# Performance work log

Measured on AMD Instinct MI355X. Metric: run time of the kernel, lower is better.

## Reference

```python
import jax, jax.numpy as jnp
import numpy as np

B, S, E = 2, 2048, 2048
H, KV, D = 16, 4, 128


def setup_inputs() -> dict:
    key = jax.random.key(0)
    k0, k1, k2, k3, k4 = jax.random.split(key, 5)
    s = 0.02  # init scale for weights
    return {
        "x": jax.random.normal(k0, (B, S, E), jnp.float32),
        "wq": jax.random.normal(k1, (E, H * D), jnp.float32) * s,
        "wk": jax.random.normal(k2, (E, KV * D), jnp.float32) * s,
        "wv": jax.random.normal(k3, (E, KV * D), jnp.float32) * s,
        "wo": jax.random.normal(k4, (H * D, E), jnp.float32) * s,
    }


def _rope_tables(seq_len, head_dim, dtype):
    inv_freq = 1.0 / (10000.0 ** (jnp.arange(0, head_dim, 2, dtype=jnp.float32) / head_dim))
    t = jnp.arange(seq_len, dtype=jnp.float32)
    freqs = jnp.outer(t, inv_freq)  # [S, D/2]
    emb = jnp.concatenate([freqs, freqs], axis=-1)  # [S, D]
    cos = jnp.cos(emb).astype(dtype)[None, None]  # [1,1,S,D]
    sin = jnp.sin(emb).astype(dtype)[None, None]
    return cos, sin


def _rotate_half(x):
    x1, x2 = jnp.split(x, 2, axis=-1)
    return jnp.concatenate([-x2, x1], axis=-1)


def reference(x, wq, wk, wv, wo):
    b, s, _ = x.shape
    # projections -> [B, heads, S, D]
    q = (x @ wq).reshape(b, s, H, D).transpose(0, 2, 1, 3)
    k = (x @ wk).reshape(b, s, KV, D).transpose(0, 2, 1, 3)
    v = (x @ wv).reshape(b, s, KV, D).transpose(0, 2, 1, 3)
    # inline RoPE (rotate-half convention), applied to q and k
    cos, sin = _rope_tables(s, D, q.dtype)
    q = q * cos + _rotate_half(q) * sin
    k = k * cos + _rotate_half(k) * sin
    # GQA: duplicate K/V heads (repeat_interleave along head dim)
    rep = H // KV
    k = jnp.repeat(k, rep, axis=1)
    v = jnp.repeat(v, rep, axis=1)
    scale = 1.0 / np.sqrt(D)
    scores = jnp.einsum('bhqd,bhkd->bhqk', q, k) * scale  # [B,H,S,S]
    attn = jax.nn.softmax(scores.astype(jnp.float32), axis=-1).astype(q.dtype)
    out = jnp.einsum('bhqk,bhkd->bhqd', attn, v)  # [B,H,S,D]
    out = out.transpose(0, 2, 1, 3).reshape(b, s, H * D)
    return out @ wo
```

## Files before the change

### kernel.cpp

```cpp
#include <hip/hip_runtime.h>
#include <hip/hip_bf16.h>

typedef __attribute__((ext_vector_type(8))) short s16x8;
typedef __attribute__((ext_vector_type(4))) float f32x4;

__device__ inline float bf2f(unsigned short u) {
  union { unsigned int i; float f; } v; v.i = ((unsigned int)u) << 16; return v.f;
}
__device__ inline unsigned short f2bf(float f) {
  union { float f; unsigned int i; } v; v.f = f;
  unsigned int r = (v.i + 0x7FFFu + ((v.i >> 16) & 1u)) >> 16;
  return (unsigned short)r;
}
__device__ inline void gl_lds16(const void* g, void* l) {
  __builtin_amdgcn_global_load_lds(
      (const __attribute__((address_space(1))) unsigned int*)g,
      (__attribute__((address_space(3))) unsigned int*)l, 16, 0, 0);
}

__global__ __launch_bounds__(256) void cast_to_bf16(const float* __restrict__ s,
                                                    unsigned short* __restrict__ d, int n4) {
  int i = blockIdx.x * 256 + threadIdx.x;
  if (i >= n4) return;
  float4 v = ((const float4*)s)[i];
  ushort4 o;
  o.x = f2bf(v.x); o.y = f2bf(v.y); o.z = f2bf(v.z); o.w = f2bf(v.w);
  ((ushort4*)d)[i] = o;
}

__global__ __launch_bounds__(256) void transpose_cast(const float* __restrict__ src,
                                                      unsigned short* __restrict__ dst,
                                                      int K, int N) {
  __shared__ float tile[32][33];
  int n0 = blockIdx.x * 32, k0 = blockIdx.y * 32;
  int tx = threadIdx.x & 31, ty = threadIdx.x >> 5;
#pragma unroll
  for (int i = 0; i < 4; ++i) {
    int k = ty + i * 8;
    tile[k][tx] = src[(size_t)(k0 + k) * N + n0 + tx];
  }
  __syncthreads();
#pragma unroll
  for (int i = 0; i < 4; ++i) {
    int n = ty + i * 8;
    dst[(size_t)(n0 + n) * K + k0 + tx] = f2bf(tile[tx][n]);
  }
}

__global__ __launch_bounds__(256) void rope_tables(float* __restrict__ ct, float* __restrict__ st) {
  int idx = blockIdx.x * 256 + threadIdx.x;
  int s = idx >> 6, i = idx & 63;
  float inv = powf(10000.0f, -(float)(2 * i) * (1.0f / 128.0f));
  float ang = (float)s * inv;
  ct[idx] = cosf(ang);
  st[idx] = sinf(ang);
}

__global__ __launch_bounds__(256) void rope_apply(unsigned short* __restrict__ qkv,
                                                  const float* __restrict__ ct,
                                                  const float* __restrict__ st) {
  int row = blockIdx.x;
  int pos = row & 2047;
  unsigned short* base = qkv + (size_t)row * 3072;
  for (int it = threadIdx.x; it < 1280; it += 256) {
    int head = it >> 6, dh = it & 63;
    int col = head < 16 ? head * 128 : 2048 + (head - 16) * 128;
    float a = bf2f(base[col + dh]);
    float b = bf2f(base[col + dh + 64]);
    float c = ct[pos * 64 + dh], sn = st[pos * 64 + dh];
    base[col + dh] = f2bf(a * c - b * sn);
    base[col + dh + 64] = f2bf(b * c + a * sn);
  }
}

__global__ __launch_bounds__(256) void vtrans(const unsigned short* __restrict__ qkv,
                                              unsigned short* __restrict__ vt) {
  __shared__ unsigned short tile[32][33];
  int tx = threadIdx.x & 31, ty = threadIdx.x >> 5;
  int s0 = blockIdx.x * 32;
  int d0 = blockIdx.y * 32;
  int bz = blockIdx.z;
  const unsigned short* src = qkv + (size_t)((bz >> 2) * 2048) * 3072 + 2560 + (bz & 3) * 128;
#pragma unroll
  for (int i = 0; i < 4; ++i)
    tile[ty + i * 8][tx] = src[(size_t)(s0 + ty + i * 8) * 3072 + d0 + tx];
  __syncthreads();
  unsigned short* dst = vt + (size_t)bz * 128 * 2048;
#pragma unroll
  for (int i = 0; i < 4; ++i)
    dst[(size_t)(d0 + ty + i * 8) * 2048 + s0 + tx] = tile[tx][ty + i * 8];
}

template <int BF16OUT>
__global__ __launch_bounds__(512, 2) void gemm256(const unsigned short* __restrict__ A,
                                                  const unsigned short* __restrict__ BT,
                                                  void* __restrict__ Cv,
                                                  int M, int N, int K) {
  __shared__ __align__(16) unsigned short Lds[2][4][256 * 32];
  const int t = threadIdx.x, lane = t & 63;
  const int wid = t >> 6, m16 = lane & 15, l4 = lane >> 4;
  const int wm = wid >> 2, wn = wid & 3;
  const int swA = (l4 ^ ((m16 >> 1) & 3)) * 16;

  int gx = gridDim.x, nwg = gx * gridDim.y;
  int wg = blockIdx.y * gx + blockIdx.x;
  if ((nwg & 7) == 0) { int q = nwg >> 3; wg = (wg & 7) * q + (wg >> 3); }
  const int rowBase = (wg / gx) * 256, colBase = (wg % gx) * 256;

  const int r0 = t >> 2, c80 = (t & 3) ^ ((r0 >> 1) & 3);
  const int g1 = 512 + t, r1 = g1 >> 2, c81 = (g1 & 3) ^ ((r1 >> 1) & 3);
  const char* pA0 = (const char*)(A + (size_t)(rowBase + r0) * K + c80 * 8);
  const char* pA1 = (const char*)(A + (size_t)(rowBase + r1) * K + c81 * 8);
  const char* pB0 = (const char*)(BT + (size_t)(colBase + r0) * K + c80 * 8);
  const char* pB1 = (const char*)(BT + (size_t)(colBase + r1) * K + c81 * 8);

  f32x4 acc[8][4];
#pragma unroll
  for (int fr = 0; fr < 8; ++fr)
#pragma unroll
    for (int fn = 0; fn < 4; ++fn) {
      f32x4 z = {0.f, 0.f, 0.f, 0.f};
      acc[fr][fn] = z;
    }
  s16x8 bf[4];

#define STG(mat, kc, kt, buf)                                             \
  {                                                                       \
    size_t ko = (size_t)((kt) * 64 + (kc) * 32) * 2;                      \
    char* pl = (char*)&Lds[buf][(mat) * 2 + (kc)][0];                     \
    gl_lds16(((mat) ? pB0 : pA0) + ko, pl + t * 16);                      \
    gl_lds16(((mat) ? pB1 : pA1) + ko, pl + 8192 + t * 16);               \
  }

#define GATE()                                         \
  asm volatile("s_waitcnt vmcnt(8)" ::: "memory");     \
  __builtin_amdgcn_s_barrier();                        \
  __builtin_amdgcn_sched_barrier(0);

#define CMP(cur, kc, frh)                                                          \
  {                                                                                \
    const char* Ap = (const char*)&Lds[cur][kc][0];                                \
    s16x8 af[4];                                                                   \
    _Pragma("unroll") for (int i = 0; i < 4; ++i)                                  \
        af[i] = *(const s16x8*)(Ap + (wm * 128 + ((frh) * 4 + i) * 16 + m16) * 64 + swA); \
    if ((frh) == 0) {                                                              \
      const char* Bp = (const char*)&Lds[cur][2 + (kc)][0];                        \
      _Pragma("unroll") for (int n = 0; n < 4; ++n)                                \
          bf[n] = *(const s16x8*)(Bp + (wn * 64 + n * 16 + m16) * 64 + swA);       \
    }                                                                              \
    __builtin_amdgcn_s_setprio(1);                                                 \
    _Pragma("unroll") for (int i = 0; i < 4; ++i)                                  \
        _Pragma("unroll") for (int n = 0; n < 4; ++n)                              \
            acc[(frh) * 4 + i][n] = __builtin_amdgcn_mfma_f32_16x16x32_bf16(       \
                af[i], bf[n], acc[(frh) * 4 + i][n], 0, 0, 0);                     \
    __builtin_amdgcn_s_setprio(0);                                                 \
  }

  const int NT = K >> 6;
  STG(0, 0, 0, 0); STG(1, 0, 0, 0);
  STG(0, 1, 0, 0); STG(1, 1, 0, 0);
  STG(0, 0, 1, 1); STG(1, 0, 1, 1);

  for (int kt = 0; kt < NT; ++kt) {
    const int cur = kt & 1;
    GATE();
    if (kt + 1 < NT) STG(0, 1, kt + 1, cur ^ 1);
    CMP(cur, 0, 0);
    __builtin_amdgcn_s_barrier();
    if (kt + 1 < NT) STG(1, 1, kt + 1, cur ^ 1);
    CMP(cur, 0, 1);
    GATE();
    if (kt + 2 < NT) STG(0, 0, kt + 2, cur);
    CMP(cur, 1, 0);
    __builtin_amdgcn_s_barrier();
    if (kt + 2 < NT) STG(1, 0, kt + 2, cur);
    CMP(cur, 1, 1);
  }
#undef STG
#undef GATE
#undef CMP

#pragma unroll
  for (int fr = 0; fr < 8; ++fr)
#pragma unroll
    for (int fn = 0; fn < 4; ++fn) {
      int rr = rowBase + wm * 128 + fr * 16 + l4 * 4;
      int cc = colBase + wn * 64 + fn * 16 + m16;
#pragma unroll
      for (int jr = 0; jr < 4; ++jr) {
        if (BF16OUT)
          ((unsigned short*)Cv)[(size_t)(rr + jr) * N + cc] = f2bf(acc[fr][fn][jr]);
        else
          ((float*)Cv)[(size_t)(rr + jr) * N + cc] = acc[fr][fn][jr];
      }
    }
}

__global__ __launch_bounds__(256, 2) void attn_kernel(const unsigned short* __restrict__ qkv,
                                                      const unsigned short* __restrict__ vt,
                                                      unsigned short* __restrict__ obuf) {
  __shared__ __align__(16) unsigned short Kl[2][64 * 128];
  __shared__ __align__(16) unsigned short Vl[2][128 * 64];
  __shared__ __align__(16) unsigned short Pl[4][16 * 64];
  const int t = threadIdx.x, lane = t & 63, w = t >> 6;
  const int m16 = lane & 15, l4 = lane >> 4;
  const int b = blockIdx.z, h = blockIdx.y, qb = blockIdx.x;
  const int kvh = h >> 2;
  const float SC = 0.08838834764831845f;
  const float THR = 90.50966799187809f;

  s16x8 qf[2][4];
  {
    const unsigned short* qp =
        qkv + (size_t)(b * 2048 + qb * 128 + w * 32 + m16) * 3072 + h * 128 + l4 * 8;
#pragma unroll
    for (int qt = 0; qt < 2; ++qt)
#pragma unroll
      for (int dc = 0; dc < 4; ++dc)
        qf[qt][dc] = *(const s16x8*)(qp + qt * 16 * 3072 + dc * 32);
  }

  float mrow[2], lsum[2];
  f32x4 acco[2][8];
#pragma unroll
  for (int qt = 0; qt < 2; ++qt) { mrow[qt] = -3e38f; lsum[qt] = 0.f; }
#pragma unroll
  for (int qt = 0; qt < 2; ++qt)
#pragma unroll
    for (int df = 0; df < 8; ++df) {
      f32x4 z = {0.f, 0.f, 0.f, 0.f};
      acco[qt][df] = z;
    }

  const char* pK[4];
  const char* pV[4];
#pragma unroll
  for (int i = 0; i < 4; ++i) {
    int c = i * 256 + t;
    {
      int row = c >> 4, ch = c & 15;
      pK[i] = (const char*)(qkv + (size_t)(b * 2048 + row) * 3072 + 2048 + kvh * 128) +
              ((ch * 16) ^ ((row & 7) << 4));
    }
    {
      int d = c >> 3, ch = c & 7;
      pV[i] = (const char*)(vt + (size_t)((b * 4 + kvh) * 128 + d) * 2048) +
              ((ch * 16) ^ ((d & 7) << 4));
    }
  }
  const size_t KADV = (size_t)64 * 3072 * 2;
  const size_t VADV = 128;

#define STAGE_T(buf)                                                         \
  {                                                                          \
    _Pragma("unroll") for (int i = 0; i < 4; ++i)                            \
        gl_lds16(pK[i], (char*)Kl[buf] + (i * 256 + t) * 16);                \
    _Pragma("unroll") for (int i = 0; i < 4; ++i)                            \
        gl_lds16(pV[i], (char*)Vl[buf] + (i * 256 + t) * 16);                \
    _Pragma("unroll") for (int i = 0; i < 4; ++i) pK[i] += KADV;             \
    _Pragma("unroll") for (int i = 0; i < 4; ++i) pV[i] += VADV;             \
  }

  int cur = 0;
  STAGE_T(0);
  __syncthreads();

  for (int kt = 0; kt < 32; ++kt) {
    if (kt < 31) STAGE_T(cur ^ 1);

    f32x4 sc[2][4];
#pragma unroll
    for (int qt = 0; qt < 2; ++qt)
#pragma unroll
      for (int kkt = 0; kkt < 4; ++kkt) {
        f32x4 z = {0.f, 0.f, 0.f, 0.f};
        sc[qt][kkt] = z;
      }
    __builtin_amdgcn_s_setprio(1);
#pragma unroll
    for (int kkt = 0; kkt < 4; ++kkt) {
      int row = kkt * 16 + m16;
      const char* kr = (const char*)Kl[cur] + row * 256;
      int sw = (row & 7) << 4;
#pragma unroll
      for (int dc = 0; dc < 4; ++dc) {
        s16x8 kf = *(const s16x8*)(kr + ((dc * 64 + l4 * 16) ^ sw));
        sc[0][kkt] = __builtin_amdgcn_mfma_f32_16x16x32_bf16(kf, qf[0][dc], sc[0][kkt], 0, 0, 0);
        sc[1][kkt] = __builtin_amdgcn_mfma_f32_16x16x32_bf16(kf, qf[1][dc], sc[1][kkt], 0, 0, 0);
      }
    }
    __builtin_amdgcn_s_setprio(0);

    float pmx[2];
    bool need = false;
#pragma unroll
    for (int qt = 0; qt < 2; ++qt) {
      float v = -3e38f;
#pragma unroll
      for (int kkt = 0; kkt < 4; ++kkt)
#pragma unroll
        for (int jr = 0; jr < 4; ++jr) v = fmaxf(v, sc[qt][kkt][jr]);
      pmx[qt] = v;
      need = need || (v > mrow[qt] + THR);
    }
    if (__any(need)) {
#pragma unroll
      for (int qt = 0; qt < 2; ++qt) {
        float pm = pmx[qt];
        pm = fmaxf(pm, __shfl_xor(pm, 16));
        pm = fmaxf(pm, __shfl_xor(pm, 32));
        float mn = fmaxf(mrow[qt], pm);
        float rs = __expf((mrow[qt] - mn) * SC);
        mrow[qt] = mn;
        lsum[qt] *= rs;
#pragma unroll
        for (int jr = 0; jr < 4; ++jr) {
          float r = __shfl(rs, l4 * 4 + jr);
#pragma unroll
          for (int df = 0; df < 8; ++df) acco[qt][df][jr] *= r;
        }
      }
    }

    s16x8 ap[2][2];
#pragma unroll
    for (int qt = 0; qt < 2; ++qt) {
      char* pr = (char*)Pl[w] + m16 * 128;
      int swp = (m16 & 7) << 4;
      float part = 0.f;
#pragma unroll
      for (int kkt = 0; kkt < 4; ++kkt) {
        float e0 = __expf((sc[qt][kkt][0] - mrow[qt]) * SC);
        float e1 = __expf((sc[qt][kkt][1] - mrow[qt]) * SC);
        float e2 = __expf((sc[qt][kkt][2] - mrow[qt]) * SC);
        float e3 = __expf((sc[qt][kkt][3] - mrow[qt]) * SC);
        part += (e0 + e1) + (e2 + e3);
        ushort4 pw;
        pw.x = f2bf(e0); pw.y = f2bf(e1); pw.z = f2bf(e2); pw.w = f2bf(e3);
        *(ushort4*)(pr + ((kkt * 32 + l4 * 8) ^ swp)) = pw;
      }
      lsum[qt] += part;
#pragma unroll
      for (int kc = 0; kc < 2; ++kc)
        ap[qt][kc] = *(const s16x8*)((const char*)Pl[w] + m16 * 128 +
                                     ((kc * 64 + l4 * 16) ^ ((m16 & 7) << 4)));
    }

    __builtin_amdgcn_s_setprio(1);
#pragma unroll
    for (int df = 0; df < 8; ++df) {
      int d = df * 16 + m16;
      const char* vr = (const char*)Vl[cur] + d * 128;
      int swv = (d & 7) << 4;
      s16x8 vf0 = *(const s16x8*)(vr + ((l4 * 16) ^ swv));
      s16x8 vf1 = *(const s16x8*)(vr + ((64 + l4 * 16) ^ swv));
      acco[0][df] = __builtin_amdgcn_mfma_f32_16x16x32_bf16(ap[0][0], vf0, acco[0][df], 0, 0, 0);
      acco[0][df] = __builtin_amdgcn_mfma_f32_16x16x32_bf16(ap[0][1], vf1, acco[0][df], 0, 0, 0);
      acco[1][df] = __builtin_amdgcn_mfma_f32_16x16x32_bf16(ap[1][0], vf0, acco[1][df], 0, 0, 0);
      acco[1][df] = __builtin_amdgcn_mfma_f32_16x16x32_bf16(ap[1][1], vf1, acco[1][df], 0, 0, 0);
    }
    __builtin_amdgcn_s_setprio(0);
    __syncthreads();
    cur ^= 1;
  }
#undef STAGE_T

#pragma unroll
  for (int qt = 0; qt < 2; ++qt) {
    float s = lsum[qt];
    s += __shfl_xor(s, 16);
    s += __shfl_xor(s, 32);
    float iv = 1.0f / s;
    unsigned short* op = obuf +
        (size_t)(b * 2048 + qb * 128 + w * 32 + qt * 16 + l4 * 4) * 2048 + h * 128 + m16;
#pragma unroll
    for (int jr = 0; jr < 4; ++jr) {
      float ivj = __shfl(iv, l4 * 4 + jr);
#pragma unroll
      for (int df = 0; df < 8; ++df)
        op[(size_t)jr * 2048 + df * 16] = f2bf(acco[qt][df][jr] * ivj);
    }
  }
}

extern "C" void kernel_launch(void* const* d_in, const int* in_sizes, int n_in,
                              void* d_out, int out_size, void* d_ws, size_t ws_size,
                              hipStream_t stream) {
  (void)in_sizes; (void)n_in; (void)out_size; (void)ws_size;
  const float* x  = (const float*)d_in[0];
  const float* wq = (const float*)d_in[1];
  const float* wk = (const float*)d_in[2];
  const float* wv = (const float*)d_in[3];
  const float* wo = (const float*)d_in[4];

  char* ws = (char*)d_ws;
  unsigned short* xb    = (unsigned short*)(ws);
  unsigned short* wqkvT = (unsigned short*)(ws + 16777216);
  unsigned short* woT   = (unsigned short*)(ws + 29360128);
  unsigned short* qkv   = (unsigned short*)(ws + 37748736);
  unsigned short* obuf  = (unsigned short*)(ws + 62914560);
  float* ct             = (float*)(ws + 79691776);
  float* st             = (float*)(ws + 80216064);
  unsigned short* vt    = xb;

  cast_to_bf16<<<8192, 256, 0, stream>>>(x, xb, 2097152);
  transpose_cast<<<dim3(64, 64), 256, 0, stream>>>(wq, wqkvT, 2048, 2048);
  transpose_cast<<<dim3(16, 64), 256, 0, stream>>>(wk, wqkvT + 2048 * 2048, 2048, 512);
  transpose_cast<<<dim3(16, 64), 256, 0, stream>>>(wv, wqkvT + 2560 * 2048, 2048, 512);
  transpose_cast<<<dim3(64, 64), 256, 0, stream>>>(wo, woT, 2048, 2048);
  rope_tables<<<512, 256, 0, stream>>>(ct, st);
  gemm256<1><<<dim3(12, 16), 512, 0, stream>>>(xb, wqkvT, qkv, 4096, 3072, 2048);
  rope_apply<<<4096, 256, 0, stream>>>(qkv, ct, st);
  vtrans<<<dim3(64, 4, 8), 256, 0, stream>>>(qkv, vt);
  attn_kernel<<<dim3(16, 16, 2), 256, 0, stream>>>(qkv, vt, obuf);
  gemm256<0><<<dim3(8, 16), 512, 0, stream>>>(obuf, woT, d_out, 4096, 2048, 2048);
}
```

Measured before the change: 233.7 us.

## Shrink attention tiles to 64 queries and 32 keys for higher occupancy

The attention kernel now gives each wave 16 query rows instead of 32 and streams K/V in 32-key tiles instead of 64. The launch grid doubles and the launch bounds ask for 4 blocks per CU. The V and P LDS swizzles are reworked for the narrower tiles, with P rows padded to 80 bytes. The goal is more resident waves and more blocks to hide latency, at the cost of less K/V reuse per block, twice as many loop iterations and barriers, and more global K/V traffic.

After: 252.8 us. 1.08x slower.

```diff
diff --git a/kernel.cpp b/kernel.cpp
--- a/kernel.cpp
+++ b/kernel.cpp
@@ -196,12 +196,12 @@
     }
 }
 
-__global__ __launch_bounds__(256, 2) void attn_kernel(const unsigned short* __restrict__ qkv,
+__global__ __launch_bounds__(256, 4) void attn_kernel(const unsigned short* __restrict__ qkv,
                                                       const unsigned short* __restrict__ vt,
                                                       unsigned short* __restrict__ obuf) {
-  __shared__ __align__(16) unsigned short Kl[2][64 * 128];
-  __shared__ __align__(16) unsigned short Vl[2][128 * 64];
-  __shared__ __align__(16) unsigned short Pl[4][16 * 64];
+  __shared__ __align__(16) unsigned short Kl[2][32 * 128];
+  __shared__ __align__(16) unsigned short Vl[2][128 * 32];
+  __shared__ __align__(16) unsigned short Pl[4][16 * 40];
   const int t = threadIdx.x, lane = t & 63, w = t >> 6;
   const int m16 = lane & 15, l4 = lane >> 4;
   const int b = blockIdx.z, h = blockIdx.y, qb = blockIdx.x;
@@ -209,33 +209,26 @@
   const float SC = 0.08838834764831845f;
   const float THR = 90.50966799187809f;
 
-  s16x8 qf[2][4];
+  s16x8 qf[4];
   {
     const unsigned short* qp =
-        qkv + (size_t)(b * 2048 + qb * 128 + w * 32 + m16) * 3072 + h * 128 + l4 * 8;
-#pragma unroll
-    for (int qt = 0; qt < 2; ++qt)
-#pragma unroll
-      for (int dc = 0; dc < 4; ++dc)
-        qf[qt][dc] = *(const s16x8*)(qp + qt * 16 * 3072 + dc * 32);
-  }
-
-  float mrow[2], lsum[2];
-  f32x4 acco[2][8];
-#pragma unroll
-  for (int qt = 0; qt < 2; ++qt) { mrow[qt] = -3e38f; lsum[qt] = 0.f; }
-#pragma unroll
-  for (int qt = 0; qt < 2; ++qt)
-#pragma unroll
-    for (int df = 0; df < 8; ++df) {
-      f32x4 z = {0.f, 0.f, 0.f, 0.f};
-      acco[qt][df] = z;
-    }
-
-  const char* pK[4];
-  const char* pV[4];
-#pragma unroll
-  for (int i = 0; i < 4; ++i) {
+        qkv + (size_t)(b * 2048 + qb * 64 + w * 16 + m16) * 3072 + h * 128 + l4 * 8;
+#pragma unroll
+    for (int dc = 0; dc < 4; ++dc) qf[dc] = *(const s16x8*)(qp + dc * 32);
+  }
+
+  float mrow = -3e38f, lsum = 0.f;
+  f32x4 acco[8];
+#pragma unroll
+  for (int df = 0; df < 8; ++df) {
+    f32x4 z = {0.f, 0.f, 0.f, 0.f};
+    acco[df] = z;
+  }
+
+  const char* pK[2];
+  const char* pV[2];
+#pragma unroll
+  for (int i = 0; i < 2; ++i) {
     int c = i * 256 + t;
     {
       int row = c >> 4, ch = c & 15;
@@ -243,121 +236,93 @@
               ((ch * 16) ^ ((row & 7) << 4));
     }
     {
-      int d = c >> 3, ch = c & 7;
+      int d = c >> 2, sl = c & 3;
       pV[i] = (const char*)(vt + (size_t)((b * 4 + kvh) * 128 + d) * 2048) +
-              ((ch * 16) ^ ((d & 7) << 4));
-    }
-  }
-  const size_t KADV = (size_t)64 * 3072 * 2;
-  const size_t VADV = 128;
+              ((sl ^ (d & 3)) * 16);
+    }
+  }
+  const size_t KADV = (size_t)32 * 3072 * 2;
+  const size_t VADV = 64;
 
 #define STAGE_T(buf)                                                         \
   {                                                                          \
-    _Pragma("unroll") for (int i = 0; i < 4; ++i)                            \
+    _Pragma("unroll") for (int i = 0; i < 2; ++i)                            \
         gl_lds16(pK[i], (char*)Kl[buf] + (i * 256 + t) * 16);                \
-    _Pragma("unroll") for (int i = 0; i < 4; ++i)                            \
+    _Pragma("unroll") for (int i = 0; i < 2; ++i)                            \
         gl_lds16(pV[i], (char*)Vl[buf] + (i * 256 + t) * 16);                \
-    _Pragma("unroll") for (int i = 0; i < 4; ++i) pK[i] += KADV;             \
-    _Pragma("unroll") for (int i = 0; i < 4; ++i) pV[i] += VADV;             \
+    _Pragma("unroll") for (int i = 0; i < 2; ++i) pK[i] += KADV;             \
+    _Pragma("unroll") for (int i = 0; i < 2; ++i) pV[i] += VADV;             \
   }
 
   int cur = 0;
   STAGE_T(0);
   __syncthreads();
 
-  for (int kt = 0; kt < 32; ++kt) {
-    if (kt < 31) STAGE_T(cur ^ 1);
-
-    f32x4 sc[2][4];
-#pragma unroll
-    for (int qt = 0; qt < 2; ++qt)
-#pragma unroll
-      for (int kkt = 0; kkt < 4; ++kkt) {
-        f32x4 z = {0.f, 0.f, 0.f, 0.f};
-        sc[qt][kkt] = z;
-      }
+  char* const prow = (char*)&Pl[w][0] + m16 * 80;
+
+  for (int kt = 0; kt < 64; ++kt) {
+    if (kt < 63) STAGE_T(cur ^ 1);
+
+    f32x4 sc2[2];
+#pragma unroll
+    for (int kkt = 0; kkt < 2; ++kkt) {
+      f32x4 z = {0.f, 0.f, 0.f, 0.f};
+      sc2[kkt] = z;
+    }
     __builtin_amdgcn_s_setprio(1);
 #pragma unroll
-    for (int kkt = 0; kkt < 4; ++kkt) {
+    for (int kkt = 0; kkt < 2; ++kkt) {
       int row = kkt * 16 + m16;
       const char* kr = (const char*)Kl[cur] + row * 256;
       int sw = (row & 7) << 4;
 #pragma unroll
       for (int dc = 0; dc < 4; ++dc) {
         s16x8 kf = *(const s16x8*)(kr + ((dc * 64 + l4 * 16) ^ sw));
-        sc[0][kkt] = __builtin_amdgcn_mfma_f32_16x16x32_bf16(kf, qf[0][dc], sc[0][kkt], 0, 0, 0);
-        sc[1][kkt] = __builtin_amdgcn_mfma_f32_16x16x32_bf16(kf, qf[1][dc], sc[1][kkt], 0, 0, 0);
+        sc2[kkt] = __builtin_amdgcn_mfma_f32_16x16x32_bf16(kf, qf[dc], sc2[kkt], 0, 0, 0);
       }
     }
     __builtin_amdgcn_s_setprio(0);
 
-    float pmx[2];
-    bool need = false;
-#pragma unroll
-    for (int qt = 0; qt < 2; ++qt) {
-      float v = -3e38f;
-#pragma unroll
-      for (int kkt = 0; kkt < 4; ++kkt)
-#pragma unroll
-        for (int jr = 0; jr < 4; ++jr) v = fmaxf(v, sc[qt][kkt][jr]);
-      pmx[qt] = v;
-      need = need || (v > mrow[qt] + THR);
-    }
-    if (__any(need)) {
-#pragma unroll
-      for (int qt = 0; qt < 2; ++qt) {
-        float pm = pmx[qt];
-        pm = fmaxf(pm, __shfl_xor(pm, 16));
-        pm = fmaxf(pm, __shfl_xor(pm, 32));
-        float mn = fmaxf(mrow[qt], pm);
-        float rs = __expf((mrow[qt] - mn) * SC);
-        mrow[qt] = mn;
-        lsum[qt] *= rs;
-#pragma unroll
-        for (int jr = 0; jr < 4; ++jr) {
-          float r = __shfl(rs, l4 * 4 + jr);
-#pragma unroll
-          for (int df = 0; df < 8; ++df) acco[qt][df][jr] *= r;
-        }
+    float v = fmaxf(fmaxf(fmaxf(sc2[0][0], sc2[0][1]), fmaxf(sc2[0][2], sc2[0][3])),
+                    fmaxf(fmaxf(sc2[1][0], sc2[1][1]), fmaxf(sc2[1][2], sc2[1][3])));
+    if (__any(v > mrow + THR)) {
+      float pm = v;
+      pm = fmaxf(pm, __shfl_xor(pm, 16));
+      pm = fmaxf(pm, __shfl_xor(pm, 32));
+      float mn = fmaxf(mrow, pm);
+      float rs = __expf((mrow - mn) * SC);
+      mrow = mn;
+      lsum *= rs;
+#pragma unroll
+      for (int jr = 0; jr < 4; ++jr) {
+        float r = __shfl(rs, l4 * 4 + jr);
+#pragma unroll
+        for (int df = 0; df < 8; ++df) acco[df][jr] *= r;
       }
     }
 
-    s16x8 ap[2][2];
-#pragma unroll
-    for (int qt = 0; qt < 2; ++qt) {
-      char* pr = (char*)Pl[w] + m16 * 128;
-      int swp = (m16 & 7) << 4;
-      float part = 0.f;
-#pragma unroll
-      for (int kkt = 0; kkt < 4; ++kkt) {
-        float e0 = __expf((sc[qt][kkt][0] - mrow[qt]) * SC);
-        float e1 = __expf((sc[qt][kkt][1] - mrow[qt]) * SC);
-        float e2 = __expf((sc[qt][kkt][2] - mrow[qt]) * SC);
-        float e3 = __expf((sc[qt][kkt][3] - mrow[qt]) * SC);
-        part += (e0 + e1) + (e2 + e3);
-        ushort4 pw;
-        pw.x = f2bf(e0); pw.y = f2bf(e1); pw.z = f2bf(e2); pw.w = f2bf(e3);
-        *(ushort4*)(pr + ((kkt * 32 + l4 * 8) ^ swp)) = pw;
-      }
-      lsum[qt] += part;
-#pragma unroll
-      for (int kc = 0; kc < 2; ++kc)
-        ap[qt][kc] = *(const s16x8*)((const char*)Pl[w] + m16 * 128 +
-                                     ((kc * 64 + l4 * 16) ^ ((m16 & 7) << 4)));
-    }
+    float part = 0.f;
+#pragma unroll
+    for (int kkt = 0; kkt < 2; ++kkt) {
+      float e0 = __expf((sc2[kkt][0] - mrow) * SC);
+      float e1 = __expf((sc2[kkt][1] - mrow) * SC);
+      float e2 = __expf((sc2[kkt][2] - mrow) * SC);
+      float e3 = __expf((sc2[kkt][3] - mrow) * SC);
+      part += (e0 + e1) + (e2 + e3);
+      ushort4 pw;
+      pw.x = f2bf(e0); pw.y = f2bf(e1); pw.z = f2bf(e2); pw.w = f2bf(e3);
+      *(ushort4*)(prow + kkt * 32 + l4 * 8) = pw;
+    }
+    lsum += part;
+    s16x8 ap = *(const s16x8*)(prow + l4 * 16);
 
     __builtin_amdgcn_s_setprio(1);
 #pragma unroll
     for (int df = 0; df < 8; ++df) {
       int d = df * 16 + m16;
-      const char* vr = (const char*)Vl[cur] + d * 128;
-      int swv = (d & 7) << 4;
-      s16x8 vf0 = *(const s16x8*)(vr + ((l4 * 16) ^ swv));
-      s16x8 vf1 = *(const s16x8*)(vr + ((64 + l4 * 16) ^ swv));
-      acco[0][df] = __builtin_amdgcn_mfma_f32_16x16x32_bf16(ap[0][0], vf0, acco[0][df], 0, 0, 0);
-      acco[0][df] = __builtin_amdgcn_mfma_f32_16x16x32_bf16(ap[0][1], vf1, acco[0][df], 0, 0, 0);
-      acco[1][df] = __builtin_amdgcn_mfma_f32_16x16x32_bf16(ap[1][0], vf0, acco[1][df], 0, 0, 0);
-      acco[1][df] = __builtin_amdgcn_mfma_f32_16x16x32_bf16(ap[1][1], vf1, acco[1][df], 0, 0, 0);
+      const char* vr = (const char*)Vl[cur] + d * 64;
+      s16x8 vf = *(const s16x8*)(vr + ((l4 * 16) ^ ((d & 3) << 4)));
+      acco[df] = __builtin_amdgcn_mfma_f32_16x16x32_bf16(ap, vf, acco[df], 0, 0, 0);
     }
     __builtin_amdgcn_s_setprio(0);
     __syncthreads();
@@ -365,20 +330,19 @@
   }
 #undef STAGE_T
 
-#pragma unroll
-  for (int qt = 0; qt < 2; ++qt) {
-    float s = lsum[qt];
+  {
+    float s = lsum;
     s += __shfl_xor(s, 16);
     s += __shfl_xor(s, 32);
     float iv = 1.0f / s;
     unsigned short* op = obuf +
-        (size_t)(b * 2048 + qb * 128 + w * 32 + qt * 16 + l4 * 4) * 2048 + h * 128 + m16;
+        (size_t)(b * 2048 + qb * 64 + w * 16 + l4 * 4) * 2048 + h * 128 + m16;
 #pragma unroll
     for (int jr = 0; jr < 4; ++jr) {
       float ivj = __shfl(iv, l4 * 4 + jr);
 #pragma unroll
       for (int df = 0; df < 8; ++df)
-        op[(size_t)jr * 2048 + df * 16] = f2bf(acco[qt][df][jr] * ivj);
+        op[(size_t)jr * 2048 + df * 16] = f2bf(acco[df][jr] * ivj);
     }
   }
 }
@@ -412,6 +376,6 @@
   gemm256<1><<<dim3(12, 16), 512, 0, stream>>>(xb, wqkvT, qkv, 4096, 3072, 2048);
   rope_apply<<<4096, 256, 0, stream>>>(qkv, ct, st);
   vtrans<<<dim3(64, 4, 8), 256, 0, stream>>>(qkv, vt);
-  attn_kernel<<<dim3(16, 16, 2), 256, 0, stream>>>(qkv, vt, obuf);
+  attn_kernel<<<dim3(32, 16, 2), 256, 0, stream>>>(qkv, vt, obuf);
   gemm256<0><<<dim3(8, 16), 512, 0, stream>>>(obuf, woT, d_out, 4096, 2048, 2048);
 }
```
